# Performance work log

Measured on AMD Instinct MI355X. Metric: run time of the kernel, lower is better.

The kernel has to match this reference:

```python
import jax, jax.numpy as jnp
import numpy as np

N = 100000   # active voxels
K = 27       # 3x3x3 kernel offsets
C = 64       # in_channels == out_channels (residual block)
EPS = 1e-5


def setup_inputs() -> dict:
    key = jax.random.key(0)
    ks = jax.random.split(key, 10)
    feats = jax.random.normal(ks[0], (N, C), dtype=jnp.float32)
    # kernel-map: for each voxel, index of the neighbor voxel for each of the 27 offsets
    nbr = jax.random.randint(ks[1], (N, K), 0, N)
    nbr = nbr.at[:, K // 2].set(jnp.arange(N))  # center offset is identity
    w_scale = 1.0 / np.sqrt(K * C)
    W1 = jax.random.normal(ks[2], (K, C, C), dtype=jnp.float32) * w_scale
    b1 = jax.random.normal(ks[3], (C,), dtype=jnp.float32) * 0.01
    g1 = jnp.ones((C,), jnp.float32)
    be1 = jnp.zeros((C,), jnp.float32)
    W2 = jax.random.normal(ks[4], (K, C, C), dtype=jnp.float32) * w_scale
    b2 = jax.random.normal(ks[5], (C,), dtype=jnp.float32) * 0.01
    g2 = jnp.ones((C,), jnp.float32)
    be2 = jnp.zeros((C,), jnp.float32)
    return {"feats": feats, "nbr": nbr, "W1": W1, "b1": b1, "g1": g1, "be1": be1,
            "W2": W2, "b2": b2, "g2": g2, "be2": be2}


def _sparse_conv(f, nbr, W, b):
    # gather neighbor features per kernel offset: [N, K, C]
    g = f[nbr]
    # per-offset matmul and reduce over offsets (gather-matmul-scatter form)
    return jnp.einsum('nkc,kcd->nd', g, W) + b


def _bn(x, gamma, beta):
    # BatchNorm over active voxels (training-mode batch stats, per channel)
    mu = x.mean(axis=0)
    var = x.var(axis=0)
    return (x - mu) * jax.lax.rsqrt(var + EPS) * gamma + beta


def reference(feats, nbr, W1, b1, g1, be1, W2, b2, g2, be2):
    h = jax.nn.relu(_bn(_sparse_conv(feats, nbr, W1, b1), g1, be1))
    h = _bn(_sparse_conv(h, nbr, W2, b2), g2, be2)
    return jax.nn.relu(h + feats)  # residual add + ReLU
```

## Files before the change

kernel.cpp:

```cpp
#include <hip/hip_runtime.h>

#define NCH 64
#define KOFF 27
#define EPSV 1e-5f

typedef __attribute__((ext_vector_type(8))) short  bf16x8;
typedef __attribute__((ext_vector_type(4))) float  f32x4;
typedef __attribute__((ext_vector_type(8))) unsigned short u16x8;

__device__ __forceinline__ unsigned short f2bf(float x) {
    unsigned int u = __float_as_uint(x);
    u += 0x7fffu + ((u >> 16) & 1u);
    return (unsigned short)(u >> 16);
}

__global__ __launch_bounds__(256)
void cast_bf16_kernel(const float* __restrict__ x, unsigned short* __restrict__ y,
                      int total8)
{
    const int idx = blockIdx.x * 256 + threadIdx.x;
    if (idx >= total8) return;
    const float4* xp = reinterpret_cast<const float4*>(x) + (size_t)idx * 2;
    const float4 a = xp[0], b = xp[1];
    u16x8 o;
    o[0] = f2bf(a.x); o[1] = f2bf(a.y); o[2] = f2bf(a.z); o[3] = f2bf(a.w);
    o[4] = f2bf(b.x); o[5] = f2bf(b.y); o[6] = f2bf(b.z); o[7] = f2bf(b.w);
    reinterpret_cast<u16x8*>(y)[idx] = o;
}

__global__ __launch_bounds__(256)
void wtrans_kernel(const float* __restrict__ W, unsigned short* __restrict__ Wt)
{
    const int t  = blockIdx.x * 256 + threadIdx.x;
    const int l  = t & 63;
    const int ct = (t >> 6) & 3;
    const int s  = (t >> 8) & 1;
    const int k  = t >> 9;
    const int d     = ct * 16 + (l & 15);
    const int cbase = s * 32 + (l >> 4) * 8;
    u16x8 o;
#pragma unroll
    for (int j = 0; j < 8; ++j)
        o[j] = f2bf(W[(size_t)k * 4096 + (size_t)(cbase + j) * 64 + d]);
    reinterpret_cast<u16x8*>(Wt)[t] = o;
}

__global__ __launch_bounds__(256, 3)
void conv_mfma_kernel(const unsigned short* __restrict__ fin,
                      const int* __restrict__ nbr,
                      const unsigned short* __restrict__ Wt,
                      const float* __restrict__ bias,
                      float* __restrict__ out, int N)
{
    __shared__ int s_idx[64 * KOFF];
    __shared__ unsigned short sA[2][64 * 72];
    __shared__ unsigned short sB[2][4096];

    const int t    = threadIdx.x;
    const int lane = t & 63;
    const int w    = t >> 6;
    const int n0   = blockIdx.x * 64;

    {
        const int* nb  = nbr + (size_t)n0 * KOFF;
        const int rem  = N - n0;
        const int maxi = (rem < 64 ? rem : 64) * KOFF;
        for (int i = t; i < 64 * KOFF; i += 256)
            s_idx[i] = (i < maxi) ? nb[i] : 0;
    }
    __syncthreads();

    auto stage = [&](int k, int b) {
#pragma unroll
        for (int h = 0; h < 2; ++h) {
            const int q = t + h * 256;
            const int v = q >> 3, p = q & 7;
            const int ridx = s_idx[v * KOFF + k];
            const uint4 d = *reinterpret_cast<const uint4*>(
                fin + (size_t)ridx * NCH + p * 8);
            *reinterpret_cast<uint4*>(&sA[b][v * 72 + p * 8]) = d;
        }
        const unsigned short* src = Wt + (size_t)k * 4096;
#pragma unroll
        for (int h = 0; h < 2; ++h) {
            const int q = t + h * 256;
            const uint4 d = *reinterpret_cast<const uint4*>(src + q * 8);
            *reinterpret_cast<uint4*>(&sB[b][q * 8]) = d;
        }
    };

    f32x4 acc[4];
#pragma unroll
    for (int ct = 0; ct < 4; ++ct) acc[ct] = (f32x4){0.f, 0.f, 0.f, 0.f};

    stage(0, 0);
    __syncthreads();

    const int m    = lane & 15;
    const int quad = lane >> 4;

    for (int k = 0; k < KOFF; ++k) {
        const int cur = k & 1;
        if (k + 1 < KOFF) stage(k + 1, cur ^ 1);

        const unsigned short* Ab = &sA[cur][(w * 16 + m) * 72 + quad * 8];
#pragma unroll
        for (int s = 0; s < 2; ++s) {
            const bf16x8 a = *reinterpret_cast<const bf16x8*>(Ab + s * 32);
#pragma unroll
            for (int ct = 0; ct < 4; ++ct) {
                const bf16x8 bb = *reinterpret_cast<const bf16x8*>(
                    &sB[cur][((s * 4 + ct) * 64 + lane) * 8]);
                acc[ct] = __builtin_amdgcn_mfma_f32_16x16x32_bf16(a, bb, acc[ct], 0, 0, 0);
            }
        }
        __syncthreads();
    }

#pragma unroll
    for (int ct = 0; ct < 4; ++ct) {
        const int ch = ct * 16 + m;
        const float bv = bias[ch];
#pragma unroll
        for (int r = 0; r < 4; ++r) {
            const int vox = n0 + w * 16 + quad * 4 + r;
            if (vox < N) out[(size_t)vox * NCH + ch] = acc[ct][r] + bv;
        }
    }
}

__global__ __launch_bounds__(256)
void stats_kernel(const float* __restrict__ x, float* __restrict__ sums, int N)
{
    __shared__ float s_s[256];
    __shared__ float s_q[256];
    const int d = threadIdx.x & 63;
    const int g = threadIdx.x >> 6;
    float s = 0.f, q = 0.f;
    for (int n = blockIdx.x * 4 + g; n < N; n += gridDim.x * 4) {
        const float v = x[(size_t)n * NCH + d];
        s += v;
        q += v * v;
    }
    s_s[threadIdx.x] = s;
    s_q[threadIdx.x] = q;
    __syncthreads();
    if (threadIdx.x < 64) {
        s = s_s[d] + s_s[64 + d] + s_s[128 + d] + s_s[192 + d];
        q = s_q[d] + s_q[64 + d] + s_q[128 + d] + s_q[192 + d];
        atomicAdd(&sums[d], s);
        atomicAdd(&sums[64 + d], q);
    }
}

__global__ __launch_bounds__(256)
void bn_relu_bf16_kernel(const float* __restrict__ x, const float* __restrict__ sums,
                         const float* __restrict__ gmm, const float* __restrict__ bet,
                         float invN, unsigned short* __restrict__ y, int total8)
{
    const int idx = blockIdx.x * 256 + threadIdx.x;
    if (idx >= total8) return;
    const int c0 = (idx & 7) * 8;
    const float4* xp = reinterpret_cast<const float4*>(x) + (size_t)idx * 2;
    const float4 a = xp[0], b = xp[1];
    float v[8] = {a.x, a.y, a.z, a.w, b.x, b.y, b.z, b.w};
    u16x8 o;
#pragma unroll
    for (int i = 0; i < 8; ++i) {
        const int c = c0 + i;
        const float mu  = sums[c] * invN;
        const float var = sums[64 + c] * invN - mu * mu;
        const float rs  = rsqrtf(var + EPSV);
        const float sc  = gmm[c] * rs;
        const float sh  = bet[c] - mu * sc;
        o[i] = f2bf(fmaxf(fmaf(v[i], sc, sh), 0.f));
    }
    reinterpret_cast<u16x8*>(y)[idx] = o;
}

__global__ __launch_bounds__(256)
void bn_res_relu_kernel(float* __restrict__ x, const float* __restrict__ feats,
                        const float* __restrict__ sums, const float* __restrict__ gmm,
                        const float* __restrict__ bet, float invN, int total4)
{
    const int idx = blockIdx.x * blockDim.x + threadIdx.x;
    if (idx >= total4) return;
    float4 v = reinterpret_cast<float4*>(x)[idx];
    const float4 f = reinterpret_cast<const float4*>(feats)[idx];
    const int c0 = (idx & 15) * 4;
    float sc[4], sh[4];
#pragma unroll
    for (int i = 0; i < 4; ++i) {
        const int c = c0 + i;
        const float mu  = sums[c] * invN;
        const float var = sums[64 + c] * invN - mu * mu;
        const float rs  = rsqrtf(var + EPSV);
        sc[i] = gmm[c] * rs;
        sh[i] = bet[c] - mu * sc[i];
    }
    v.x = fmaxf(fmaf(v.x, sc[0], sh[0]) + f.x, 0.f);
    v.y = fmaxf(fmaf(v.y, sc[1], sh[1]) + f.y, 0.f);
    v.z = fmaxf(fmaf(v.z, sc[2], sh[2]) + f.z, 0.f);
    v.w = fmaxf(fmaf(v.w, sc[3], sh[3]) + f.w, 0.f);
    reinterpret_cast<float4*>(x)[idx] = v;
}

extern "C" void kernel_launch(void* const* d_in, const int* in_sizes, int n_in,
                              void* d_out, int out_size, void* d_ws, size_t ws_size,
                              hipStream_t stream)
{
    const float* feats = (const float*)d_in[0];
    const int*   nbr   = (const int*)d_in[1];
    const float* W1    = (const float*)d_in[2];
    const float* b1    = (const float*)d_in[3];
    const float* g1    = (const float*)d_in[4];
    const float* be1   = (const float*)d_in[5];
    const float* W2    = (const float*)d_in[6];
    const float* b2    = (const float*)d_in[7];
    const float* g2    = (const float*)d_in[8];
    const float* be2   = (const float*)d_in[9];
    float* out = (float*)d_out;

    const int N  = in_sizes[0] / NCH;
    const int NC = N * NCH;
    const float invN = 1.0f / (float)N;

    float*          h0   = (float*)d_ws;
    unsigned short* fbf  = (unsigned short*)(h0 + NC);
    unsigned short* hbf  = fbf + NC;
    unsigned short* wt1  = hbf + NC;
    unsigned short* wt2  = wt1 + KOFF * 4096;
    float*          stat = (float*)(wt2 + KOFF * 4096);

    hipMemsetAsync(stat, 0, 256 * sizeof(float), stream);

    const int total8   = NC / 8;
    const int castGrid = (total8 + 255) / 256;
    const int convGrid = (N + 63) / 64;
    const int ewGrid   = (NC / 4 + 255) / 256;

    cast_bf16_kernel<<<castGrid, 256, 0, stream>>>(feats, fbf, total8);
    wtrans_kernel<<<KOFF * 512 / 256, 256, 0, stream>>>(W1, wt1);
    wtrans_kernel<<<KOFF * 512 / 256, 256, 0, stream>>>(W2, wt2);

    conv_mfma_kernel<<<convGrid, 256, 0, stream>>>(fbf, nbr, wt1, b1, h0, N);
    stats_kernel<<<512, 256, 0, stream>>>(h0, stat, N);
    bn_relu_bf16_kernel<<<castGrid, 256, 0, stream>>>(h0, stat, g1, be1, invN,
                                                      hbf, total8);
    conv_mfma_kernel<<<convGrid, 256, 0, stream>>>(hbf, nbr, wt2, b2, out, N);
    stats_kernel<<<512, 256, 0, stream>>>(out, stat + 128, N);
    bn_res_relu_kernel<<<ewGrid, 256, 0, stream>>>(out, feats, stat + 128, g2, be2,
                                                   invN, NC / 4);
}
```

Measured before the change: 311.4 us.

## Fuse BN stats into conv epilogue, single-wave register-pipelined conv, merge prep kernels

The conv kernel becomes a single 64-thread wave per 64-voxel tile. It loads gathered features and weights straight from global memory into registers with double buffering, which drops the LDS staging and block barriers. Per-channel sum and sum-of-squares are reduced in the conv epilogue with shuffles and atomics, so the two separate stats passes over the fp32 outputs go away. The memset, feature cast and both weight transposes are merged into one prep kernel to cut launches. In exchange, each wave holds a lot of register state (16 accumulators plus double-buffered A/B), weight tiles are reloaded from global or cache by every wave, and the atomic count rises with the block count.

```diff
diff --git a/kernel.cpp b/kernel.cpp
--- a/kernel.cpp
+++ b/kernel.cpp
@@ -15,142 +15,147 @@
 }
 
 __global__ __launch_bounds__(256)
-void cast_bf16_kernel(const float* __restrict__ x, unsigned short* __restrict__ y,
-                      int total8)
-{
-    const int idx = blockIdx.x * 256 + threadIdx.x;
+void prep_kernel(const float* __restrict__ feats,
+                 const float* __restrict__ W1, const float* __restrict__ W2,
+                 unsigned short* __restrict__ fbf,
+                 unsigned short* __restrict__ wt1, unsigned short* __restrict__ wt2,
+                 float* __restrict__ stat, int total8)
+{
+    const int b = blockIdx.x;
+    if (b == 0) {
+        stat[threadIdx.x] = 0.f;
+        return;
+    }
+    if (b <= 108) {
+        const float* W = (b <= 54) ? W1 : W2;
+        unsigned short* Wt = (b <= 54) ? wt1 : wt2;
+        const int t = (b <= 54 ? b - 1 : b - 55) * 256 + threadIdx.x;
+        const int l  = t & 63;
+        const int ct = (t >> 6) & 3;
+        const int s  = (t >> 8) & 1;
+        const int k  = t >> 9;
+        const int d     = ct * 16 + (l & 15);
+        const int cbase = s * 32 + (l >> 4) * 8;
+        u16x8 o;
+#pragma unroll
+        for (int j = 0; j < 8; ++j)
+            o[j] = f2bf(W[(size_t)k * 4096 + (size_t)(cbase + j) * 64 + d]);
+        reinterpret_cast<u16x8*>(Wt)[t] = o;
+        return;
+    }
+    const int idx = (b - 109) * 256 + threadIdx.x;
     if (idx >= total8) return;
-    const float4* xp = reinterpret_cast<const float4*>(x) + (size_t)idx * 2;
-    const float4 a = xp[0], b = xp[1];
+    const float4* xp = reinterpret_cast<const float4*>(feats) + (size_t)idx * 2;
+    const float4 a = xp[0], c = xp[1];
     u16x8 o;
     o[0] = f2bf(a.x); o[1] = f2bf(a.y); o[2] = f2bf(a.z); o[3] = f2bf(a.w);
-    o[4] = f2bf(b.x); o[5] = f2bf(b.y); o[6] = f2bf(b.z); o[7] = f2bf(b.w);
-    reinterpret_cast<u16x8*>(y)[idx] = o;
-}
-
-__global__ __launch_bounds__(256)
-void wtrans_kernel(const float* __restrict__ W, unsigned short* __restrict__ Wt)
-{
-    const int t  = blockIdx.x * 256 + threadIdx.x;
-    const int l  = t & 63;
-    const int ct = (t >> 6) & 3;
-    const int s  = (t >> 8) & 1;
-    const int k  = t >> 9;
-    const int d     = ct * 16 + (l & 15);
-    const int cbase = s * 32 + (l >> 4) * 8;
-    u16x8 o;
-#pragma unroll
-    for (int j = 0; j < 8; ++j)
-        o[j] = f2bf(W[(size_t)k * 4096 + (size_t)(cbase + j) * 64 + d]);
-    reinterpret_cast<u16x8*>(Wt)[t] = o;
-}
-
-__global__ __launch_bounds__(256, 3)
+    o[4] = f2bf(c.x); o[5] = f2bf(c.y); o[6] = f2bf(c.z); o[7] = f2bf(c.w);
+    reinterpret_cast<u16x8*>(fbf)[idx] = o;
+}
+
+__global__ __launch_bounds__(64, 2)
 void conv_mfma_kernel(const unsigned short* __restrict__ fin,
                       const int* __restrict__ nbr,
                       const unsigned short* __restrict__ Wt,
                       const float* __restrict__ bias,
-                      float* __restrict__ out, int N)
-{
-    __shared__ int s_idx[64 * KOFF];
-    __shared__ unsigned short sA[2][64 * 72];
-    __shared__ unsigned short sB[2][4096];
-
-    const int t    = threadIdx.x;
-    const int lane = t & 63;
-    const int w    = t >> 6;
+                      float* __restrict__ out, float* __restrict__ stat, int N)
+{
+    __shared__ int s_idx[KOFF * 64 + 64];
+
+    const int lane = threadIdx.x;
     const int n0   = blockIdx.x * 64;
+    const int m    = lane & 15;
+    const int quad = lane >> 4;
 
     {
-        const int* nb  = nbr + (size_t)n0 * KOFF;
         const int rem  = N - n0;
         const int maxi = (rem < 64 ? rem : 64) * KOFF;
-        for (int i = t; i < 64 * KOFF; i += 256)
-            s_idx[i] = (i < maxi) ? nb[i] : 0;
-    }
-    __syncthreads();
-
-    auto stage = [&](int k, int b) {
-#pragma unroll
-        for (int h = 0; h < 2; ++h) {
-            const int q = t + h * 256;
-            const int v = q >> 3, p = q & 7;
-            const int ridx = s_idx[v * KOFF + k];
-            const uint4 d = *reinterpret_cast<const uint4*>(
-                fin + (size_t)ridx * NCH + p * 8);
-            *reinterpret_cast<uint4*>(&sA[b][v * 72 + p * 8]) = d;
+        const int* nb  = nbr + (size_t)n0 * KOFF;
+#pragma unroll
+        for (int j = 0; j < KOFF; ++j) {
+            const int p = j * 64 + lane;
+            s_idx[p] = (p < maxi) ? nb[p] : 0;
         }
-        const unsigned short* src = Wt + (size_t)k * 4096;
-#pragma unroll
-        for (int h = 0; h < 2; ++h) {
-            const int q = t + h * 256;
-            const uint4 d = *reinterpret_cast<const uint4*>(src + q * 8);
-            *reinterpret_cast<uint4*>(&sB[b][q * 8]) = d;
-        }
-    };
-
-    f32x4 acc[4];
-#pragma unroll
-    for (int ct = 0; ct < 4; ++ct) acc[ct] = (f32x4){0.f, 0.f, 0.f, 0.f};
-
-    stage(0, 0);
-    __syncthreads();
-
-    const int m    = lane & 15;
-    const int quad = lane >> 4;
-
-    for (int k = 0; k < KOFF; ++k) {
-        const int cur = k & 1;
-        if (k + 1 < KOFF) stage(k + 1, cur ^ 1);
-
-        const unsigned short* Ab = &sA[cur][(w * 16 + m) * 72 + quad * 8];
-#pragma unroll
-        for (int s = 0; s < 2; ++s) {
-            const bf16x8 a = *reinterpret_cast<const bf16x8*>(Ab + s * 32);
-#pragma unroll
-            for (int ct = 0; ct < 4; ++ct) {
-                const bf16x8 bb = *reinterpret_cast<const bf16x8*>(
-                    &sB[cur][((s * 4 + ct) * 64 + lane) * 8]);
-                acc[ct] = __builtin_amdgcn_mfma_f32_16x16x32_bf16(a, bb, acc[ct], 0, 0, 0);
-            }
-        }
-        __syncthreads();
-    }
+    }
+
+    f32x4 acc[4][4];
+#pragma unroll
+    for (int mt = 0; mt < 4; ++mt)
+#pragma unroll
+        for (int ct = 0; ct < 4; ++ct) acc[mt][ct] = (f32x4){0.f, 0.f, 0.f, 0.f};
+
+    bf16x8 A[2][4][2];
+    bf16x8 B[2][2][4];
+
+#define LOADK(k, p)                                                          \
+    {                                                                        \
+        _Pragma("unroll")                                                    \
+        for (int mt = 0; mt < 4; ++mt) {                                     \
+            const int r = s_idx[(mt * 16 + m) * KOFF + (k)];                 \
+            const unsigned short* fp = fin + (size_t)r * NCH + quad * 8;     \
+            A[p][mt][0] = *reinterpret_cast<const bf16x8*>(fp);              \
+            A[p][mt][1] = *reinterpret_cast<const bf16x8*>(fp + 32);         \
+        }                                                                    \
+        const unsigned short* wp = Wt + (size_t)(k) * 4096 + lane * 8;       \
+        _Pragma("unroll")                                                    \
+        for (int s = 0; s < 2; ++s)                                          \
+            _Pragma("unroll")                                                \
+            for (int ct = 0; ct < 4; ++ct)                                   \
+                B[p][s][ct] =                                                \
+                    *reinterpret_cast<const bf16x8*>(wp + (s * 4 + ct) * 512);\
+    }
+
+#define DOMFMA(p)                                                            \
+    {                                                                        \
+        _Pragma("unroll")                                                    \
+        for (int mt = 0; mt < 4; ++mt)                                       \
+            _Pragma("unroll")                                                \
+            for (int s = 0; s < 2; ++s)                                      \
+                _Pragma("unroll")                                            \
+                for (int ct = 0; ct < 4; ++ct)                               \
+                    acc[mt][ct] = __builtin_amdgcn_mfma_f32_16x16x32_bf16(   \
+                        A[p][mt][s], B[p][s][ct], acc[mt][ct], 0, 0, 0);     \
+    }
+
+    LOADK(0, 0);
+#pragma unroll 1
+    for (int k = 0; k < KOFF - 1; k += 2) {
+        LOADK(k + 1, 1);
+        DOMFMA(0);
+        LOADK(k + 2, 0);
+        DOMFMA(1);
+    }
+    DOMFMA(0);
 
 #pragma unroll
     for (int ct = 0; ct < 4; ++ct) {
         const int ch = ct * 16 + m;
         const float bv = bias[ch];
-#pragma unroll
-        for (int r = 0; r < 4; ++r) {
-            const int vox = n0 + w * 16 + quad * 4 + r;
-            if (vox < N) out[(size_t)vox * NCH + ch] = acc[ct][r] + bv;
+        float s = 0.f, q = 0.f;
+#pragma unroll
+        for (int mt = 0; mt < 4; ++mt) {
+#pragma unroll
+            for (int r = 0; r < 4; ++r) {
+                const int vox = n0 + mt * 16 + quad * 4 + r;
+                if (vox < N) {
+                    const float v = acc[mt][ct][r] + bv;
+                    out[(size_t)vox * NCH + ch] = v;
+                    s += v;
+                    q += v * v;
+                }
+            }
         }
-    }
-}
-
-__global__ __launch_bounds__(256)
-void stats_kernel(const float* __restrict__ x, float* __restrict__ sums, int N)
-{
-    __shared__ float s_s[256];
-    __shared__ float s_q[256];
-    const int d = threadIdx.x & 63;
-    const int g = threadIdx.x >> 6;
-    float s = 0.f, q = 0.f;
-    for (int n = blockIdx.x * 4 + g; n < N; n += gridDim.x * 4) {
-        const float v = x[(size_t)n * NCH + d];
-        s += v;
-        q += v * v;
-    }
-    s_s[threadIdx.x] = s;
-    s_q[threadIdx.x] = q;
-    __syncthreads();
-    if (threadIdx.x < 64) {
-        s = s_s[d] + s_s[64 + d] + s_s[128 + d] + s_s[192 + d];
-        q = s_q[d] + s_q[64 + d] + s_q[128 + d] + s_q[192 + d];
-        atomicAdd(&sums[d], s);
-        atomicAdd(&sums[64 + d], q);
-    }
+        s += __shfl_xor(s, 16, 64);
+        s += __shfl_xor(s, 32, 64);
+        q += __shfl_xor(q, 16, 64);
+        q += __shfl_xor(q, 32, 64);
+        if (quad == 0) {
+            atomicAdd(&stat[ch], s);
+            atomicAdd(&stat[64 + ch], q);
+        }
+    }
+#undef LOADK
+#undef DOMFMA
 }
 
 __global__ __launch_bounds__(256)
@@ -232,23 +237,18 @@
     unsigned short* wt2  = wt1 + KOFF * 4096;
     float*          stat = (float*)(wt2 + KOFF * 4096);
 
-    hipMemsetAsync(stat, 0, 256 * sizeof(float), stream);
-
     const int total8   = NC / 8;
     const int castGrid = (total8 + 255) / 256;
+    const int prepGrid = 1 + 108 + castGrid;
     const int convGrid = (N + 63) / 64;
-    const int ewGrid   = (NC / 4 + 255) / 256;
-
-    cast_bf16_kernel<<<castGrid, 256, 0, stream>>>(feats, fbf, total8);
-    wtrans_kernel<<<KOFF * 512 / 256, 256, 0, stream>>>(W1, wt1);
-    wtrans_kernel<<<KOFF * 512 / 256, 256, 0, stream>>>(W2, wt2);
-
-    conv_mfma_kernel<<<convGrid, 256, 0, stream>>>(fbf, nbr, wt1, b1, h0, N);
-    stats_kernel<<<512, 256, 0, stream>>>(h0, stat, N);
+
+    prep_kernel<<<prepGrid, 256, 0, stream>>>(feats, W1, W2, fbf, wt1, wt2,
+                                              stat, total8);
+    conv_mfma_kernel<<<convGrid, 64, 0, stream>>>(fbf, nbr, wt1, b1, h0, stat, N);
     bn_relu_bf16_kernel<<<castGrid, 256, 0, stream>>>(h0, stat, g1, be1, invN,
                                                       hbf, total8);
-    conv_mfma_kernel<<<convGrid, 256, 0, stream>>>(hbf, nbr, wt2, b2, out, N);
-    stats_kernel<<<512, 256, 0, stream>>>(out, stat + 128, N);
-    bn_res_relu_kernel<<<ewGrid, 256, 0, stream>>>(out, feats, stat + 128, g2, be2,
-                                                   invN, NC / 4);
-}
+    conv_mfma_kernel<<<convGrid, 64, 0, stream>>>(hbf, nbr, wt2, b2, out,
+                                                  stat + 128, N);
+    bn_res_relu_kernel<<<(NC / 4 + 255) / 256, 256, 0, stream>>>(
+        out, feats, stat + 128, g2, be2, invN, NC / 4);
+}
```

Measured after the change: 322.8 us. 3.7% more time.
